# Kernel tuning notes

Hardware: AMD Instinct MI355X
Metric: run time of the kernel (lower is better)

The kernel has to match this reference:

```python
import jax, jax.numpy as jnp
import numpy as np

MARGIN = 1.0


def setup_inputs() -> dict:
    key = jax.random.key(0)
    k1, k2, k3 = jax.random.split(key, 3)
    n, d = 8192, 128
    feat1 = jax.random.normal(k1, (n, d), dtype=jnp.float32)
    feat2 = jax.random.normal(k2, (n, d), dtype=jnp.float32)
    # similarity labels in {+1, -1}, as expected by HingeEmbeddingLoss
    simi = (2 * jax.random.randint(k3, (n, n), 0, 2) - 1).astype(jnp.int32)
    return {"feat1": feat1, "feat2": feat2, "simi": simi}


def reference(feat1, feat2, simi):
    # logits[i,j] = -||feat1_i - feat2_j||^2, computed without the O(n*m*d) expand
    sq1 = jnp.sum(feat1 * feat1, axis=-1, keepdims=True)          # [n, 1]
    sq2 = jnp.sum(feat2 * feat2, axis=-1)                          # [m]
    cross = jnp.einsum('nd,md->nm', feat1, feat2)                  # [n, m]
    logits = -(sq1 + sq2[None, :] - 2.0 * cross)                   # [n, m]
    probs = jax.nn.softmax(logits, axis=1)                         # [n, m]
    # HingeEmbeddingLoss: x if y==1 else max(0, margin - x); mean reduction
    loss = jnp.where(simi == 1, probs, jnp.maximum(0.0, MARGIN - probs))
    return jnp.mean(loss)
```

## Files before the change

kernel.cpp:

```cpp
#include <hip/hip_runtime.h>
#include <hip/hip_bf16.h>
#include <stdint.h>

#define N 8192
#define D 128
#define NCHUNK 16
#define CHUNK (N / NCHUNK)
#define RT 128
#define CT 64
#define NTILES (CHUNK / CT)
#define NBLK (N / RT * NCHUNK)

typedef short bf16x8 __attribute__((ext_vector_type(8)));
typedef float f32x4 __attribute__((ext_vector_type(4)));
typedef int   i32x4 __attribute__((ext_vector_type(4)));
typedef unsigned int uint32;

#define OFF_ACC   0u
#define OFF_SQ2   1024u
#define OFF_BCNT  (OFF_SQ2 + N * 4u)
#define OFF_M     (OFF_BCNT + NBLK * 4u)
#define OFF_L     (OFF_M + NCHUNK * N * 4u)
#define OFF_S     (OFF_L + NCHUNK * N * 4u)
#define OFF_F1    (OFF_S + NCHUNK * N * 4u)
#define OFF_F2    (OFF_F1 + N * D * 2u)

__global__ __launch_bounds__(256)
void prep_kernel(const float* __restrict__ f1, const float* __restrict__ f2,
                 unsigned short* __restrict__ f1b, unsigned short* __restrict__ f2b,
                 float* __restrict__ sq2) {
    const int w    = blockIdx.x * 4 + (threadIdx.x >> 6);
    const int lane = threadIdx.x & 63;
    for (int row = w; row < N; row += 1024) {
        float a0 = f1[row * D + lane];
        float a1 = f1[row * D + 64 + lane];
        float b0 = f2[row * D + lane];
        float b1 = f2[row * D + 64 + lane];
        __hip_bfloat16 t;
        t = __float2bfloat16(a0); f1b[row * D + lane]      = *(unsigned short*)&t;
        t = __float2bfloat16(a1); f1b[row * D + 64 + lane] = *(unsigned short*)&t;
        t = __float2bfloat16(b0); f2b[row * D + lane]      = *(unsigned short*)&t;
        t = __float2bfloat16(b1); f2b[row * D + 64 + lane] = *(unsigned short*)&t;
        float ss = b0 * b0 + b1 * b1;
        #pragma unroll
        for (int off = 32; off > 0; off >>= 1) ss += __shfl_xor(ss, off);
        if (lane == 0) sq2[row] = ss;
    }
}

__global__ __launch_bounds__(256)
void main_kernel(const unsigned short* __restrict__ f1b,
                 const unsigned short* __restrict__ f2b,
                 const float* __restrict__ sq2,
                 const int* __restrict__ simi,
                 float* __restrict__ pm, float* __restrict__ pl, float* __restrict__ ps,
                 uint32* __restrict__ blockcnt) {
    __shared__ unsigned short ldsB[2][CT * D];
    __shared__ uint32 cred[4];

    const int tid  = threadIdx.x;
    const int wave = tid >> 6;
    const int lane = tid & 63;
    const int lo   = lane & 15;
    const int hi   = lane >> 4;

    const int rowtile = blockIdx.x;
    const int chunk   = blockIdx.y;
    const int rbase   = rowtile * RT + wave * 32;
    const int cbase0  = chunk * CHUNK;

    bf16x8 afrag[2][4];
    #pragma unroll
    for (int a = 0; a < 2; a++) {
        const unsigned short* ap = f1b + (size_t)(rbase + a * 16 + lo) * D + hi * 8;
        #pragma unroll
        for (int kk = 0; kk < 4; kk++)
            afrag[a][kk] = *reinterpret_cast<const bf16x8*>(ap + kk * 32);
    }

    const int sq_ = (tid >> 4);
    const int sg_ = tid & 15;

    const int* simi_p = simi + (size_t)(rbase + hi * 4) * N + cbase0 + 4 * lo;

    float m[2][4], l[2][4], s[2][4];
    #pragma unroll
    for (int a = 0; a < 2; a++)
        #pragma unroll
        for (int r = 0; r < 4; r++) { m[a][r] = -1e30f; l[a][r] = 0.f; s[a][r] = 0.f; }
    uint32 cnt = 0;

    #pragma unroll
    for (int it = 0; it < 4; it++) {
        int q = it * 16 + sq_;
        int c = 4 * (q & 15) + (q >> 4);
        uint4 v = *reinterpret_cast<const uint4*>(f2b + (size_t)(cbase0 + c) * D + sg_ * 8);
        *reinterpret_cast<uint4*>(&ldsB[0][q * D + ((sg_ ^ (q & 15)) * 8)]) = v;
    }
    __syncthreads();

    for (int t = 0; t < NTILES; t++) {
        const int cur = t & 1;

        i32x4 mkv[2][4];
        #pragma unroll
        for (int a = 0; a < 2; a++)
            #pragma unroll
            for (int r = 0; r < 4; r++)
                mkv[a][r] = __builtin_nontemporal_load(
                    reinterpret_cast<const i32x4*>(simi_p + (size_t)(a * 16 + r) * N));

        uint4 stg[4];
        if (t < NTILES - 1) {
            const int cb_n = cbase0 + (t + 1) * CT;
            #pragma unroll
            for (int it = 0; it < 4; it++) {
                int q = it * 16 + sq_;
                int c = 4 * (q & 15) + (q >> 4);
                stg[it] = *reinterpret_cast<const uint4*>(
                    f2b + (size_t)(cb_n + c) * D + sg_ * 8);
            }
        }

        f32x4 acc[2][4];
        #pragma unroll
        for (int cf = 0; cf < 4; cf++) {
            acc[0][cf] = (f32x4){0.f, 0.f, 0.f, 0.f};
            acc[1][cf] = (f32x4){0.f, 0.f, 0.f, 0.f};
            const int brow = cf * 16 + lo;
            #pragma unroll
            for (int kk = 0; kk < 4; kk++) {
                int g = kk * 4 + hi;
                bf16x8 b = *reinterpret_cast<const bf16x8*>(
                    &ldsB[cur][brow * D + ((g ^ (brow & 15)) * 8)]);
                acc[0][cf] = __builtin_amdgcn_mfma_f32_16x16x32_bf16(afrag[0][kk], b, acc[0][cf], 0, 0, 0);
                acc[1][cf] = __builtin_amdgcn_mfma_f32_16x16x32_bf16(afrag[1][kk], b, acc[1][cf], 0, 0, 0);
            }
        }
        __builtin_amdgcn_sched_barrier(0);

        uint32 mb[2][4];
        #pragma unroll
        for (int a = 0; a < 2; a++)
            #pragma unroll
            for (int r = 0; r < 4; r++) {
                i32x4 v = mkv[a][r];
                uint32 nib = (uint32)(v[0] == 1) | ((uint32)(v[1] == 1) << 1) |
                             ((uint32)(v[2] == 1) << 2) | ((uint32)(v[3] == 1) << 3);
                mb[a][r] = nib;
                cnt += 4u - __popc(nib);
            }

        f32x4 sqv = *reinterpret_cast<const f32x4*>(sq2 + cbase0 + t * CT + 4 * lo);
        #pragma unroll
        for (int a = 0; a < 2; a++)
            #pragma unroll
            for (int r = 0; r < 4; r++) {
                float lg[4];
                #pragma unroll
                for (int cf = 0; cf < 4; cf++)
                    lg[cf] = 2.0f * acc[a][cf][r] - sqv[cf];
                float tm = fmaxf(fmaxf(lg[0], lg[1]), fmaxf(lg[2], lg[3]));
                float mn = fmaxf(m[a][r], tm);
                float al = __expf(m[a][r] - mn);
                m[a][r] = mn;
                float p[4];
                #pragma unroll
                for (int cf = 0; cf < 4; cf++) p[cf] = __expf(lg[cf] - mn);
                l[a][r] = l[a][r] * al + ((p[0] + p[1]) + (p[2] + p[3]));
                float sm = 0.f;
                #pragma unroll
                for (int cf = 0; cf < 4; cf++)
                    sm += ((mb[a][r] >> cf) & 1u) ? p[cf] : 0.f;
                s[a][r] = s[a][r] * al + sm;
            }

        if (t < NTILES - 1) {
            #pragma unroll
            for (int it = 0; it < 4; it++) {
                int q = it * 16 + sq_;
                *reinterpret_cast<uint4*>(
                    &ldsB[cur ^ 1][q * D + ((sg_ ^ (q & 15)) * 8)]) = stg[it];
            }
        }

        __syncthreads();
        simi_p += CT;
    }

    #pragma unroll
    for (int a = 0; a < 2; a++)
        #pragma unroll
        for (int r = 0; r < 4; r++) {
            float M = m[a][r];
            #pragma unroll
            for (int off = 1; off < 16; off <<= 1)
                M = fmaxf(M, __shfl_xor(M, off));
            float sc = __expf(m[a][r] - M);
            float L = l[a][r] * sc, S = s[a][r] * sc;
            #pragma unroll
            for (int off = 1; off < 16; off <<= 1) {
                L += __shfl_xor(L, off);
                S += __shfl_xor(S, off);
            }
            if (lo == 0) {
                int row = rbase + a * 16 + hi * 4 + r;
                int idx = chunk * N + row;
                pm[idx] = M; pl[idx] = L; ps[idx] = S;
            }
        }

    #pragma unroll
    for (int off = 1; off < 64; off <<= 1) cnt += __shfl_xor(cnt, off);
    if (lane == 0) cred[wave] = cnt;
    __syncthreads();
    if (tid == 0)
        blockcnt[blockIdx.y * 64 + blockIdx.x] = cred[0] + cred[1] + cred[2] + cred[3];
}

__global__ void merge_kernel(const float* __restrict__ pm, const float* __restrict__ pl,
                             const float* __restrict__ ps, const uint32* __restrict__ blockcnt,
                             float* __restrict__ s_acc, uint32* __restrict__ neg_acc) {
    const int row = blockIdx.x * 256 + threadIdx.x;
    float M = -1e30f;
    #pragma unroll
    for (int k = 0; k < NCHUNK; k++) M = fmaxf(M, pm[k * N + row]);
    float L = 0.f, S = 0.f;
    #pragma unroll
    for (int k = 0; k < NCHUNK; k++) {
        float e = __expf(pm[k * N + row] - M);
        L += pl[k * N + row] * e;
        S += ps[k * N + row] * e;
    }
    float r = S / L;
    uint32 pc = (threadIdx.x < 32) ? blockcnt[blockIdx.x * 32 + threadIdx.x] : 0u;
    #pragma unroll
    for (int off = 32; off > 0; off >>= 1) {
        r  += __shfl_xor(r, off);
        pc += __shfl_xor(pc, off);
    }
    __shared__ float red[4];
    __shared__ uint32 redp[4];
    int lane = threadIdx.x & 63, w = threadIdx.x >> 6;
    if (lane == 0) { red[w] = r; redp[w] = pc; }
    __syncthreads();
    if (threadIdx.x == 0) {
        atomicAdd(s_acc, red[0] + red[1] + red[2] + red[3]);
        atomicAdd(neg_acc, redp[0] + redp[1] + redp[2] + redp[3]);
    }
}

__global__ void final_kernel(const float* __restrict__ s_acc, const uint32* __restrict__ neg_acc,
                             float* __restrict__ out) {
    double S = (double)s_acc[0];
    double C = (double)neg_acc[0];
    double n = (double)N;
    out[0] = (float)((2.0 * S + C - n) / (n * n));
}

extern "C" void kernel_launch(void* const* d_in, const int* in_sizes, int n_in,
                              void* d_out, int out_size, void* d_ws, size_t ws_size,
                              hipStream_t stream) {
    const float* f1   = (const float*)d_in[0];
    const float* f2   = (const float*)d_in[1];
    const int*   simi = (const int*)d_in[2];
    float* out = (float*)d_out;
    char* ws = (char*)d_ws;

    float*  acc_s    = (float*)(ws + OFF_ACC);
    uint32* acc_n    = (uint32*)(ws + OFF_ACC + 4);
    float*  sq2      = (float*)(ws + OFF_SQ2);
    uint32* blockcnt = (uint32*)(ws + OFF_BCNT);
    float*  pm       = (float*)(ws + OFF_M);
    float*  pl       = (float*)(ws + OFF_L);
    float*  ps       = (float*)(ws + OFF_S);
    unsigned short* f1b = (unsigned short*)(ws + OFF_F1);
    unsigned short* f2b = (unsigned short*)(ws + OFF_F2);

    hipMemsetAsync(ws + OFF_ACC, 0, 64, stream);
    prep_kernel<<<256, 256, 0, stream>>>(f1, f2, f1b, f2b, sq2);
    main_kernel<<<dim3(N / RT, NCHUNK), 256, 0, stream>>>(f1b, f2b, sq2, simi,
                                                          pm, pl, ps, blockcnt);
    merge_kernel<<<N / 256, 256, 0, stream>>>(pm, pl, ps, blockcnt, acc_s, acc_n);
    final_kernel<<<1, 1, 0, stream>>>(acc_s, acc_n, out);
}
```

Measured before the change: 390.5 us.

## Use direct global-to-LDS loads, prefetch simi one tile ahead, base-2 softmax

Replaces the register-staged copy of feat2 tiles into LDS with direct global_load_lds transfers, and prefetches the next tile's similarity labels a full iteration ahead so their latency overlaps the MFMA work. It also caches the scaled squared norms for the chunk in LDS and folds log2(e) into the logits so the softmax can use native exp2. The prep kernel switches to vectorized float2 loads. The LDS swizzle and the sync placement change, which risks race or layout mismatches, and the extra prefetched registers may raise register pressure.

```diff
diff --git a/kernel.cpp b/kernel.cpp
--- a/kernel.cpp
+++ b/kernel.cpp
@@ -11,10 +11,16 @@
 #define NTILES (CHUNK / CT)
 #define NBLK (N / RT * NCHUNK)
 
+#define LOG2E     1.4426950408889634f
+#define TWO_LOG2E 2.8853900817779268f
+
 typedef short bf16x8 __attribute__((ext_vector_type(8)));
 typedef float f32x4 __attribute__((ext_vector_type(4)));
 typedef int   i32x4 __attribute__((ext_vector_type(4)));
 typedef unsigned int uint32;
+
+#define AS1 __attribute__((address_space(1)))
+#define AS3 __attribute__((address_space(3)))
 
 #define OFF_ACC   0u
 #define OFF_SQ2   1024u
@@ -32,16 +38,15 @@
     const int w    = blockIdx.x * 4 + (threadIdx.x >> 6);
     const int lane = threadIdx.x & 63;
     for (int row = w; row < N; row += 1024) {
-        float a0 = f1[row * D + lane];
-        float a1 = f1[row * D + 64 + lane];
-        float b0 = f2[row * D + lane];
-        float b1 = f2[row * D + 64 + lane];
-        __hip_bfloat16 t;
-        t = __float2bfloat16(a0); f1b[row * D + lane]      = *(unsigned short*)&t;
-        t = __float2bfloat16(a1); f1b[row * D + 64 + lane] = *(unsigned short*)&t;
-        t = __float2bfloat16(b0); f2b[row * D + lane]      = *(unsigned short*)&t;
-        t = __float2bfloat16(b1); f2b[row * D + 64 + lane] = *(unsigned short*)&t;
-        float ss = b0 * b0 + b1 * b1;
+        float2 a = *reinterpret_cast<const float2*>(f1 + row * D + 2 * lane);
+        float2 b = *reinterpret_cast<const float2*>(f2 + row * D + 2 * lane);
+        __hip_bfloat16 a0 = __float2bfloat16(a.x), a1 = __float2bfloat16(a.y);
+        __hip_bfloat16 b0 = __float2bfloat16(b.x), b1 = __float2bfloat16(b.y);
+        ushort2 ua = make_ushort2(*(unsigned short*)&a0, *(unsigned short*)&a1);
+        ushort2 ub = make_ushort2(*(unsigned short*)&b0, *(unsigned short*)&b1);
+        *reinterpret_cast<ushort2*>(f1b + row * D + 2 * lane) = ua;
+        *reinterpret_cast<ushort2*>(f2b + row * D + 2 * lane) = ub;
+        float ss = b.x * b.x + b.y * b.y;
         #pragma unroll
         for (int off = 32; off > 0; off >>= 1) ss += __shfl_xor(ss, off);
         if (lane == 0) sq2[row] = ss;
@@ -56,6 +61,7 @@
                  float* __restrict__ pm, float* __restrict__ pl, float* __restrict__ ps,
                  uint32* __restrict__ blockcnt) {
     __shared__ unsigned short ldsB[2][CT * D];
+    __shared__ float sq2l[CHUNK];
     __shared__ uint32 cred[4];
 
     const int tid  = threadIdx.x;
@@ -78,8 +84,8 @@
             afrag[a][kk] = *reinterpret_cast<const bf16x8*>(ap + kk * 32);
     }
 
-    const int sq_ = (tid >> 4);
-    const int sg_ = tid & 15;
+    const int whi = wave * 4 + hi;
+    const int sgx = lo ^ whi;
 
     const int* simi_p = simi + (size_t)(rbase + hi * 4) * N + cbase0 + 4 * lo;
 
@@ -92,35 +98,56 @@
 
     #pragma unroll
     for (int it = 0; it < 4; it++) {
-        int q = it * 16 + sq_;
-        int c = 4 * (q & 15) + (q >> 4);
-        uint4 v = *reinterpret_cast<const uint4*>(f2b + (size_t)(cbase0 + c) * D + sg_ * 8);
-        *reinterpret_cast<uint4*>(&ldsB[0][q * D + ((sg_ ^ (q & 15)) * 8)]) = v;
-    }
+        const unsigned short* gp =
+            f2b + (size_t)(cbase0 + 16 * wave + 4 * hi + it) * D + sgx * 8;
+        unsigned short* lp = &ldsB[0][(it * 16 + wave * 4) * D];
+        __builtin_amdgcn_global_load_lds((const AS1 void*)gp, (AS3 void*)lp, 16, 0, 0);
+    }
+    i32x4 mkv[2][4];
+    #pragma unroll
+    for (int a = 0; a < 2; a++)
+        #pragma unroll
+        for (int r = 0; r < 4; r++)
+            mkv[a][r] = __builtin_nontemporal_load(
+                reinterpret_cast<const i32x4*>(simi_p + (size_t)(a * 16 + r) * N));
+    #pragma unroll
+    for (int i = 0; i < 2; i++)
+        sq2l[tid + i * 256] = LOG2E * sq2[cbase0 + tid + i * 256];
     __syncthreads();
 
     for (int t = 0; t < NTILES; t++) {
         const int cur = t & 1;
 
-        i32x4 mkv[2][4];
+        uint32 mb[2][4];
         #pragma unroll
         for (int a = 0; a < 2; a++)
             #pragma unroll
-            for (int r = 0; r < 4; r++)
-                mkv[a][r] = __builtin_nontemporal_load(
-                    reinterpret_cast<const i32x4*>(simi_p + (size_t)(a * 16 + r) * N));
-
-        uint4 stg[4];
+            for (int r = 0; r < 4; r++) {
+                i32x4 v = mkv[a][r];
+                uint32 nib = (uint32)(v[0] == 1) | ((uint32)(v[1] == 1) << 1) |
+                             ((uint32)(v[2] == 1) << 2) | ((uint32)(v[3] == 1) << 3);
+                mb[a][r] = nib;
+                cnt += 4u - __popc(nib);
+            }
+
         if (t < NTILES - 1) {
+            const int* sp = simi_p + (size_t)(t + 1) * CT;
+            #pragma unroll
+            for (int a = 0; a < 2; a++)
+                #pragma unroll
+                for (int r = 0; r < 4; r++)
+                    mkv[a][r] = __builtin_nontemporal_load(
+                        reinterpret_cast<const i32x4*>(sp + (size_t)(a * 16 + r) * N));
             const int cb_n = cbase0 + (t + 1) * CT;
             #pragma unroll
             for (int it = 0; it < 4; it++) {
-                int q = it * 16 + sq_;
-                int c = 4 * (q & 15) + (q >> 4);
-                stg[it] = *reinterpret_cast<const uint4*>(
-                    f2b + (size_t)(cb_n + c) * D + sg_ * 8);
+                const unsigned short* gp =
+                    f2b + (size_t)(cb_n + 16 * wave + 4 * hi + it) * D + sgx * 8;
+                unsigned short* lp = &ldsB[cur ^ 1][(it * 16 + wave * 4) * D];
+                __builtin_amdgcn_global_load_lds((const AS1 void*)gp, (AS3 void*)lp, 16, 0, 0);
             }
         }
+        __builtin_amdgcn_sched_barrier(0);
 
         f32x4 acc[2][4];
         #pragma unroll
@@ -137,21 +164,8 @@
                 acc[1][cf] = __builtin_amdgcn_mfma_f32_16x16x32_bf16(afrag[1][kk], b, acc[1][cf], 0, 0, 0);
             }
         }
-        __builtin_amdgcn_sched_barrier(0);
-
-        uint32 mb[2][4];
-        #pragma unroll
-        for (int a = 0; a < 2; a++)
-            #pragma unroll
-            for (int r = 0; r < 4; r++) {
-                i32x4 v = mkv[a][r];
-                uint32 nib = (uint32)(v[0] == 1) | ((uint32)(v[1] == 1) << 1) |
-                             ((uint32)(v[2] == 1) << 2) | ((uint32)(v[3] == 1) << 3);
-                mb[a][r] = nib;
-                cnt += 4u - __popc(nib);
-            }
-
-        f32x4 sqv = *reinterpret_cast<const f32x4*>(sq2 + cbase0 + t * CT + 4 * lo);
+
+        f32x4 sqv = *reinterpret_cast<const f32x4*>(&sq2l[t * CT + 4 * lo]);
         #pragma unroll
         for (int a = 0; a < 2; a++)
             #pragma unroll
@@ -159,14 +173,15 @@
                 float lg[4];
                 #pragma unroll
                 for (int cf = 0; cf < 4; cf++)
-                    lg[cf] = 2.0f * acc[a][cf][r] - sqv[cf];
+                    lg[cf] = TWO_LOG2E * acc[a][cf][r] - sqv[cf];
                 float tm = fmaxf(fmaxf(lg[0], lg[1]), fmaxf(lg[2], lg[3]));
                 float mn = fmaxf(m[a][r], tm);
-                float al = __expf(m[a][r] - mn);
+                float al = __builtin_amdgcn_exp2f(m[a][r] - mn);
                 m[a][r] = mn;
                 float p[4];
                 #pragma unroll
-                for (int cf = 0; cf < 4; cf++) p[cf] = __expf(lg[cf] - mn);
+                for (int cf = 0; cf < 4; cf++)
+                    p[cf] = __builtin_amdgcn_exp2f(lg[cf] - mn);
                 l[a][r] = l[a][r] * al + ((p[0] + p[1]) + (p[2] + p[3]));
                 float sm = 0.f;
                 #pragma unroll
@@ -175,17 +190,7 @@
                 s[a][r] = s[a][r] * al + sm;
             }
 
-        if (t < NTILES - 1) {
-            #pragma unroll
-            for (int it = 0; it < 4; it++) {
-                int q = it * 16 + sq_;
-                *reinterpret_cast<uint4*>(
-                    &ldsB[cur ^ 1][q * D + ((sg_ ^ (q & 15)) * 8)]) = stg[it];
-            }
-        }
-
-        __syncthreads();
-        simi_p += CT;
+        if (t < NTILES - 1) __syncthreads();
     }
 
     #pragma unroll
@@ -196,7 +201,7 @@
             #pragma unroll
             for (int off = 1; off < 16; off <<= 1)
                 M = fmaxf(M, __shfl_xor(M, off));
-            float sc = __expf(m[a][r] - M);
+            float sc = __builtin_amdgcn_exp2f(m[a][r] - M);
             float L = l[a][r] * sc, S = s[a][r] * sc;
             #pragma unroll
             for (int off = 1; off < 16; off <<= 1) {
@@ -228,7 +233,7 @@
     float L = 0.f, S = 0.f;
     #pragma unroll
     for (int k = 0; k < NCHUNK; k++) {
-        float e = __expf(pm[k * N + row] - M);
+        float e = __builtin_amdgcn_exp2f(pm[k * N + row] - M);
         L += pl[k * N + row] * e;
         S += ps[k * N + row] * e;
     }
```

New measurement: 382.9 us. Within noise of the previous version (-1.9%).
